# Optimization experiments

Hardware: AMD Instinct MI355X
Metric: run time of the kernel (lower is better)

Reference implementation:

```python
import jax, jax.numpy as jnp
import numpy as np
import math

B, T, C, H = 2, 2048, 1024, 16
HD = C // H  # head_dim = 64
SCALE = 1.0 / math.sqrt(HD)


def _e8_head_dirs(n_heads: int) -> np.ndarray:
    # Type-1 E8 roots in original generation order: (+-1 at i, +-1 at j), i<j,
    # sign order (-1,-1),(-1,1),(1,-1),(1,1); then L2-normalized (norm sqrt(2)).
    roots = []
    for i in range(8):
        for j in range(i + 1, 8):
            for si in (-1.0, 1.0):
                for sj in (-1.0, 1.0):
                    r = np.zeros(8, dtype=np.float32)
                    r[i] = si
                    r[j] = sj
                    roots.append(r)
    roots = np.stack(roots)  # [112, 8], first n_heads used
    roots = roots / np.linalg.norm(roots, axis=1, keepdims=True)
    return roots[:n_heads]


def setup_inputs() -> dict:
    key = jax.random.key(0)
    k1, k2, k3, k4 = jax.random.split(key, 4)
    x = jax.random.normal(k1, (B, T, C), dtype=jnp.float32)
    # nn.Linear-style init scale
    w_qkv = jax.random.normal(k2, (C, 3 * C), dtype=jnp.float32) * (1.0 / math.sqrt(C))
    w_out = jax.random.normal(k3, (C, C), dtype=jnp.float32) * (1.0 / math.sqrt(C))
    head_scales = jax.random.normal(k4, (H,), dtype=jnp.float32) * 0.1
    head_dirs = jnp.asarray(_e8_head_dirs(H))  # [H, 8] buffer (not trained)
    return {"x": x, "w_qkv": w_qkv, "w_out": w_out,
            "head_scales": head_scales, "head_dirs": head_dirs}


def reference(x, w_qkv, w_out, head_scales, head_dirs):
    Bx, Tx, Cx = x.shape
    qkv = (x @ w_qkv).reshape(Bx, Tx, 3, H, HD)
    qkv = jnp.transpose(qkv, (2, 0, 3, 1, 4))  # [3, B, H, T, HD]
    q, k, v = qkv[0], qkv[1], qkv[2]
    scores = jnp.einsum('bhqd,bhkd->bhqk', q, k) * SCALE  # [B,H,T,T]
    causal = jnp.tril(jnp.ones((Tx, Tx), dtype=bool))
    scores = jnp.where(causal[None, None], scores, -jnp.inf)
    # E8 geometric bias: rank-1 per-head bias from projections onto root dirs
    q_proj = jnp.einsum('bhtd,hd->bht', q[..., :8], head_dirs)
    k_proj = jnp.einsum('bhtd,hd->bht', k[..., :8], head_dirs)
    geo_bias = q_proj[..., :, None] * k_proj[..., None, :]  # [B,H,T,T]
    scores = scores + head_scales[None, :, None, None] * geo_bias
    attn = jax.nn.softmax(scores, axis=-1)
    out = jnp.einsum('bhqk,bhkd->bhqd', attn, v)  # [B,H,T,HD]
    out = jnp.transpose(out, (0, 2, 1, 3)).reshape(Bx, Tx, Cx)
    return out @ w_out
```

## Files before the change

kernel.cpp:

```cpp
#include <hip/hip_runtime.h>
#include <stdint.h>


typedef float f32x4 __attribute__((ext_vector_type(4)));
typedef unsigned short u16x8 __attribute__((ext_vector_type(8)));
typedef unsigned short u16x4 __attribute__((ext_vector_type(4)));
typedef unsigned int u32x2 __attribute__((ext_vector_type(2)));
typedef __bf16 bf16x8 __attribute__((ext_vector_type(8)));

static __device__ __forceinline__ unsigned short f2bf(float f) {
  unsigned u = __float_as_uint(f);
  u += 0x7FFFu + ((u >> 16) & 1u);
  return (unsigned short)(u >> 16);
}
static __device__ __forceinline__ float bf2f(unsigned short s) {
  return __uint_as_float(((unsigned)s) << 16);
}
static __device__ __forceinline__ f32x4 mfma16(u16x8 a, u16x8 b, f32x4 c) {
  return __builtin_amdgcn_mfma_f32_16x16x32_bf16(
      __builtin_bit_cast(bf16x8, a), __builtin_bit_cast(bf16x8, b), c, 0, 0, 0);
}
static __device__ __forceinline__ unsigned cvtpk(float lo, float hi) {
  unsigned d;
  asm("v_cvt_pk_bf16_f32 %0, %1, %2" : "=v"(d) : "v"(lo), "v"(hi));
  return d;
}

#define GLD16(gp, lp) __builtin_amdgcn_global_load_lds( \
    (const __attribute__((address_space(1))) unsigned int*)(gp), \
    (__attribute__((address_space(3))) unsigned int*)(lp), 16, 0, 0)

__global__ __launch_bounds__(256) void k_prep(const float* __restrict__ x,
                                              const float* __restrict__ wqkv,
                                              const float* __restrict__ wout,
                                              unsigned short* __restrict__ xb,
                                              unsigned short* __restrict__ wqkvT,
                                              unsigned short* __restrict__ woutT) {
  __shared__ float t[64][65];
  const int bid = blockIdx.x;
  if (bid < 4096) {
    int i = bid * 256 + threadIdx.x;
    f32x4 v = *(const f32x4*)(x + (size_t)i * 4);
    u16x4 o;
#pragma unroll
    for (int j = 0; j < 4; ++j) o[j] = f2bf(v[j]);
    *(u16x4*)(xb + (size_t)i * 4) = o;
    return;
  }
  const float* in;
  unsigned short* out;
  int Cc, bx, by;
  if (bid < 4864) {
    int tt = bid - 4096;
    in = wqkv; out = wqkvT; Cc = 3072;
    bx = tt % 48; by = tt / 48;
  } else {
    int tt = bid - 4864;
    in = wout; out = woutT; Cc = 1024;
    bx = tt & 15; by = tt >> 4;
  }
  const int R = 1024;
  int tr = by * 64, tc = bx * 64;
  int tx = threadIdx.x & 15, ty = threadIdx.x >> 4;
#pragma unroll
  for (int i = 0; i < 4; ++i) {
    int rr = ty + i * 16;
    f32x4 v = *(const f32x4*)(in + (size_t)(tr + rr) * Cc + tc + tx * 4);
#pragma unroll
    for (int j = 0; j < 4; ++j) t[rr][tx * 4 + j] = v[j];
  }
  __syncthreads();
#pragma unroll
  for (int i = 0; i < 4; ++i) {
    int cc = ty + i * 16;
    int rr = tx * 4;
    u16x4 o;
#pragma unroll
    for (int j = 0; j < 4; ++j) o[j] = f2bf(t[rr + j][cc]);
    *(u16x4*)(out + (size_t)(tc + cc) * R + tr + rr) = o;
  }
}

__global__ __launch_bounds__(256) void k_gemm_qkv(const unsigned short* __restrict__ A,
                                                  const unsigned short* __restrict__ Bt,
                                                  unsigned short* __restrict__ qo,
                                                  unsigned short* __restrict__ ko,
                                                  unsigned short* __restrict__ vTo) {
  __shared__ unsigned short lA[128 * 64];
  __shared__ unsigned short lB[128 * 64];
  const int tid = threadIdx.x;
  const int lane = tid & 63, wid = tid >> 6;
  const int wr = wid >> 1, wc = wid & 1;
  const int r = lane & 15, g = lane >> 4;
  const int mbase = blockIdx.y * 128;
  const int nbase = blockIdx.x * 128;
  const int rsw = (r & 7) << 4;

  f32x4 acc[4][4] = {};

  for (int kt = 0; kt < 16; ++kt) {
    __syncthreads();
#pragma unroll
    for (int p = 0; p < 4; ++p) {
      int L = p * 4096 + tid * 16;
      int row = L >> 7;
      int cb = (L >> 4) & 7;
      int cbg = cb ^ (row & 7);
      GLD16(A + (size_t)(mbase + row) * 1024 + kt * 64 + cbg * 8, lA + (L >> 1));
      GLD16(Bt + (size_t)(nbase + row) * 1024 + kt * 64 + cbg * 8, lB + (L >> 1));
    }
    __syncthreads();
#pragma unroll
    for (int s = 0; s < 2; ++s) {
      u16x8 af[4], bfv[4];
      const int csw = (s * 64 + g * 16) ^ rsw;
#pragma unroll
      for (int m = 0; m < 4; ++m)
        af[m] = *(const u16x8*)((const char*)lA + (wr * 64 + m * 16 + r) * 128 + csw);
#pragma unroll
      for (int n = 0; n < 4; ++n)
        bfv[n] = *(const u16x8*)((const char*)lB + (wc * 64 + n * 16 + r) * 128 + csw);
#pragma unroll
      for (int m = 0; m < 4; ++m)
#pragma unroll
        for (int n = 0; n < 4; ++n) acc[m][n] = mfma16(af[m], bfv[n], acc[m][n]);
    }
  }

#pragma unroll
  for (int m = 0; m < 4; ++m) {
#pragma unroll
    for (int n = 0; n < 4; ++n) {
      int ng = nbase + wc * 64 + n * 16 + r;
      int m0 = mbase + wr * 64 + m * 16 + g * 4;
      int sec = ng >> 10, rem = ng & 1023, hh = rem >> 6, d = rem & 63;
      int b = m0 >> 11, t0 = m0 & 2047;
      size_t bh = (size_t)(b * 16 + hh);
      if (sec == 2) {
        u16x4 o;
#pragma unroll
        for (int e = 0; e < 4; ++e) o[e] = f2bf(acc[m][n][e]);
        *(u16x4*)(vTo + (bh * 64 + d) * 2048 + t0) = o;
      } else {
        unsigned short* dst = (sec == 0 ? qo : ko);
#pragma unroll
        for (int e = 0; e < 4; ++e)
          dst[(bh * 2048 + t0 + e) * 64 + d] = f2bf(acc[m][n][e]);
      }
    }
  }
}

__global__ __launch_bounds__(256) void k_gout(const unsigned short* __restrict__ A,
                                              const unsigned short* __restrict__ Bt,
                                              float* __restrict__ fo) {
  __shared__ unsigned short lA[128 * 64];
  __shared__ unsigned short lB[64 * 64];
  const int tid = threadIdx.x;
  const int lane = tid & 63, wid = tid >> 6;
  const int wr = wid >> 1, wc = wid & 1;
  const int r = lane & 15, g = lane >> 4;
  const int mbase = blockIdx.y * 128;
  const int nbase = blockIdx.x * 64;
  const int rsw = (r & 7) << 4;

  f32x4 acc[4][2] = {};

  for (int kt = 0; kt < 16; ++kt) {
    __syncthreads();
#pragma unroll
    for (int p = 0; p < 4; ++p) {
      int L = p * 4096 + tid * 16;
      int row = L >> 7;
      int cb = (L >> 4) & 7;
      int cbg = cb ^ (row & 7);
      GLD16(A + (size_t)(mbase + row) * 1024 + kt * 64 + cbg * 8, lA + (L >> 1));
      if (p < 2)
        GLD16(Bt + (size_t)(nbase + row) * 1024 + kt * 64 + cbg * 8, lB + (L >> 1));
    }
    __syncthreads();
#pragma unroll
    for (int s = 0; s < 2; ++s) {
      u16x8 af[4], bfv[2];
      const int csw = (s * 64 + g * 16) ^ rsw;
#pragma unroll
      for (int m = 0; m < 4; ++m)
        af[m] = *(const u16x8*)((const char*)lA + (wr * 64 + m * 16 + r) * 128 + csw);
#pragma unroll
      for (int n = 0; n < 2; ++n)
        bfv[n] = *(const u16x8*)((const char*)lB + (wc * 32 + n * 16 + r) * 128 + csw);
#pragma unroll
      for (int m = 0; m < 4; ++m)
#pragma unroll
        for (int n = 0; n < 2; ++n) acc[m][n] = mfma16(af[m], bfv[n], acc[m][n]);
    }
  }

#pragma unroll
  for (int m = 0; m < 4; ++m)
#pragma unroll
    for (int n = 0; n < 2; ++n) {
      int ng = nbase + wc * 32 + n * 16 + r;
      int m0 = mbase + wr * 64 + m * 16 + g * 4;
#pragma unroll
      for (int e = 0; e < 4; ++e)
        fo[(size_t)(m0 + e) * 1024 + ng] = acc[m][n][e];
    }
}

__global__ __launch_bounds__(256, 4) void k_attn(const unsigned short* __restrict__ qb,
                                                 const unsigned short* __restrict__ kb,
                                                 const unsigned short* __restrict__ vTb,
                                                 const float* __restrict__ hsc,
                                                 const float* __restrict__ hdir,
                                                 unsigned short* __restrict__ o2) {
  __shared__ unsigned short lK[2][64 * 64];
  __shared__ unsigned short lV[2][64 * 64];
  __shared__ unsigned short lP[4][16 * 64];

  const int tid = threadIdx.x, lane = tid & 63, wid = tid >> 6;
  const int r = lane & 15, g = lane >> 4;
  const int bid = blockIdx.x;
  const int u = bid & 255, kq = bid >> 8;
  const int bh = u & 31, j = u >> 5;
  const int a = (kq == 0) ? j : (kq == 1) ? (31 - j) : (kq == 2) ? (8 + j) : (23 - j);
  const int nk = a + 1;
  const int qbase = a * 64;
  const int h = bh & 15, bi = bh >> 4;

  const size_t kbase = (size_t)bh * (2048 * 64);
  const size_t vbase = (size_t)bh * (64 * 2048);

  const int L0 = tid * 16, L1 = 4096 + tid * 16;
  const int sr0 = L0 >> 7, sr1 = L1 >> 7;
  const int sc0 = ((L0 >> 4) & 7) ^ (sr0 & 7);
  const int sc1 = ((L1 >> 4) & 7) ^ (sr1 & 7);
  const unsigned short* kG0 = kb + kbase + (size_t)sr0 * 64 + sc0 * 8;
  const unsigned short* kG1 = kb + kbase + (size_t)sr1 * 64 + sc1 * 8;
  const unsigned short* vG0 = vTb + vbase + (size_t)sr0 * 2048 + sc0 * 8;
  const unsigned short* vG1 = vTb + vbase + (size_t)sr1 * 2048 + sc1 * 8;
  unsigned short* const dK0a = (unsigned short*)lK[0] + (L0 >> 1);
  unsigned short* const dK0b = (unsigned short*)lK[0] + (L1 >> 1);
  unsigned short* const dK1a = (unsigned short*)lK[1] + (L0 >> 1);
  unsigned short* const dK1b = (unsigned short*)lK[1] + (L1 >> 1);
  unsigned short* const dV0a = (unsigned short*)lV[0] + (L0 >> 1);
  unsigned short* const dV0b = (unsigned short*)lV[0] + (L1 >> 1);
  unsigned short* const dV1a = (unsigned short*)lV[1] + (L0 >> 1);
  unsigned short* const dV1b = (unsigned short*)lV[1] + (L1 >> 1);

#define ATTN_STAGE(B) do {                        \
    GLD16(kG0, dK##B##a); GLD16(kG1, dK##B##b);   \
    GLD16(vG0, dV##B##a); GLD16(vG1, dV##B##b);   \
    kG0 += 4096; kG1 += 4096; vG0 += 64; vG1 += 64; } while (0)

  ATTN_STAGE(0);

  const float LOG2E = 1.44269504088896f;
  const float hs = hsc[h];
  float dir8[8];
#pragma unroll
  for (int j2 = 0; j2 < 8; ++j2) dir8[j2] = hdir[h * 8 + j2];

  u16x8 qc0, qc1;
  {
    const unsigned short* qrow = qb + ((size_t)bh * 2048 + qbase + wid * 16 + r) * 64;
    float proj = 0.f;
    u16x8 qv = *(const u16x8*)qrow;
#pragma unroll
    for (int j2 = 0; j2 < 8; ++j2) proj += bf2f(qv[j2]) * dir8[j2];
#pragma unroll
    for (int s = 0; s < 2; ++s) {
      u16x8 raw = *(const u16x8*)(qrow + s * 32 + g * 8);
      u16x8 ov;
#pragma unroll
      for (int j2 = 0; j2 < 8; ++j2) {
        float v = bf2f(raw[j2]) * (0.125f * LOG2E);
        if (s == 0 && g == 0) v += (hs * LOG2E) * proj * dir8[j2];
        ov[j2] = f2bf(v);
      }
      if (s == 0) qc0 = ov; else qc1 = ov;
    }
  }

  const int swz = (r & 7) << 4;
  const u16x8* kp[2][8];
  const u16x8* vp[2][8];
#pragma unroll
  for (int b = 0; b < 2; ++b) {
    const char* kc = (const char*)lK[b];
    const char* vc = (const char*)lV[b];
#pragma unroll
    for (int ct = 0; ct < 4; ++ct) {
      int krow = ct * 16 + r, sw = (krow & 7) << 4;
      kp[b][ct * 2 + 0] = (const u16x8*)(kc + krow * 128 + ((g * 16) ^ sw));
      kp[b][ct * 2 + 1] = (const u16x8*)(kc + krow * 128 + ((64 + g * 16) ^ sw));
    }
#pragma unroll
    for (int s = 0; s < 2; ++s)
#pragma unroll
      for (int dt = 0; dt < 4; ++dt) {
        int dd = dt * 16 + r;
        vp[b][s * 4 + dt] = (const u16x8*)(vc + dd * 128 + ((s * 64 + g * 16) ^ ((dd & 7) << 4)));
      }
  }
  unsigned short* pw = &lP[wid][0];
  u32x2* pwr[4];
  const u16x8* prd[2];
#pragma unroll
  for (int ct = 0; ct < 4; ++ct)
    pwr[ct] = (u32x2*)((char*)pw + r * 128 + ((ct * 32 + g * 8) ^ swz));
#pragma unroll
  for (int s = 0; s < 2; ++s)
    prd[s] = (const u16x8*)((const char*)pw + r * 128 + ((s * 64 + g * 16) ^ swz));

  f32x4 accO[4] = {};
  float lp = 0.f;
  const int qq = qbase + wid * 16 + r;

  asm volatile("s_waitcnt vmcnt(0)" ::: "memory");
  __builtin_amdgcn_sched_barrier(0);
  __builtin_amdgcn_s_barrier();

#define ATTN_BODY(B, KT) do {                                                  \
    f32x4 accS[4];                                                             \
    __builtin_amdgcn_s_setprio(1);                                             \
    _Pragma("unroll")                                                          \
    for (int ct = 0; ct < 4; ++ct) {                                           \
      f32x4 s4 = {0.f, 0.f, 0.f, 0.f};                                         \
      s4 = mfma16(*kp[B][ct * 2 + 0], qc0, s4);                                \
      s4 = mfma16(*kp[B][ct * 2 + 1], qc1, s4);                                \
      accS[ct] = s4;                                                           \
    }                                                                          \
    __builtin_amdgcn_s_setprio(0);                                             \
    if ((KT) == nk - 1) {                                                      \
      _Pragma("unroll")                                                        \
      for (int ct = 0; ct < 4; ++ct)                                           \
        _Pragma("unroll")                                                      \
        for (int e = 0; e < 4; ++e) {                                          \
          int kk = (KT) * 64 + ct * 16 + g * 4 + e;                            \
          if (kk > qq) accS[ct][e] = -1e30f;                                   \
        }                                                                      \
    }                                                                          \
    float p[4][4];                                                             \
    _Pragma("unroll")                                                          \
    for (int ct = 0; ct < 4; ++ct)                                             \
      _Pragma("unroll")                                                        \
      for (int e = 0; e < 4; ++e) p[ct][e] = exp2f(accS[ct][e]);               \
    _Pragma("unroll")                                                          \
    for (int ct = 0; ct < 4; ++ct)                                             \
      lp += (p[ct][0] + p[ct][1]) + (p[ct][2] + p[ct][3]);                     \
    _Pragma("unroll")                                                          \
    for (int ct = 0; ct < 4; ++ct) {                                           \
      u32x2 w;                                                                 \
      w[0] = cvtpk(p[ct][0], p[ct][1]);                                        \
      w[1] = cvtpk(p[ct][2], p[ct][3]);                                        \
      *pwr[ct] = w;                                                            \
    }                                                                          \
    asm volatile("s_waitcnt lgkmcnt(0)" ::: "memory");                         \
    __builtin_amdgcn_sched_barrier(0);                                         \
    __builtin_amdgcn_s_setprio(1);                                             \
    _Pragma("unroll")                                                          \
    for (int s = 0; s < 2; ++s) {                                              \
      u16x8 pa = *prd[s];                                                      \
      _Pragma("unroll")                                                        \
      for (int dt = 0; dt < 4; ++dt)                                           \
        accO[dt] = mfma16(*vp[B][s * 4 + dt], pa, accO[dt]);                   \
    }                                                                          \
    __builtin_amdgcn_s_setprio(0);                                             \
  } while (0)

#define ATTN_SYNC() do {                                  \
    asm volatile("s_waitcnt vmcnt(0)" ::: "memory");      \
    __builtin_amdgcn_sched_barrier(0);                    \
    __builtin_amdgcn_s_barrier(); } while (0)

  int kt = 0;
  for (;;) {
    if (kt + 1 < nk) ATTN_STAGE(1);
    ATTN_BODY(0, kt);
    ++kt; if (kt == nk) break;
    ATTN_SYNC();
    if (kt + 1 < nk) ATTN_STAGE(0);
    ATTN_BODY(1, kt);
    ++kt; if (kt == nk) break;
    ATTN_SYNC();
  }
#undef ATTN_BODY
#undef ATTN_STAGE
#undef ATTN_SYNC

  lp += __shfl_xor(lp, 16, 64);
  lp += __shfl_xor(lp, 32, 64);
  float inv = 1.f / lp;
#pragma unroll
  for (int dt = 0; dt < 4; ++dt) {
    u16x4 o;
#pragma unroll
    for (int e = 0; e < 4; ++e) o[e] = f2bf(accO[dt][e] * inv);
    *(u16x4*)(o2 + ((size_t)(bi * 2048 + qq)) * 1024 + h * 64 + dt * 16 + g * 4) = o;
  }
}

extern "C" void kernel_launch(void* const* d_in, const int* in_sizes, int n_in,
                              void* d_out, int out_size, void* d_ws, size_t ws_size,
                              hipStream_t stream) {
  const float* x    = (const float*)d_in[0];
  const float* wqkv = (const float*)d_in[1];
  const float* wout = (const float*)d_in[2];
  const float* hsc  = (const float*)d_in[3];
  const float* hdir = (const float*)d_in[4];
  float* outp = (float*)d_out;

  char* ws = (char*)d_ws;
  unsigned short* xb    = (unsigned short*)(ws + 0);
  unsigned short* wqkvT = (unsigned short*)(ws + 8388608);
  unsigned short* woutT = (unsigned short*)(ws + 14680064);
  unsigned short* qb    = (unsigned short*)(ws + 16777216);
  unsigned short* kb    = (unsigned short*)(ws + 25165824);
  unsigned short* vT    = (unsigned short*)(ws + 33554432);
  unsigned short* x2b   = (unsigned short*)(ws + 41943040);
  if (ws_size < 50331648u) return;

  k_prep<<<5120, 256, 0, stream>>>(x, wqkv, wout, xb, wqkvT, woutT);
  k_gemm_qkv<<<dim3(24, 32), 256, 0, stream>>>(xb, wqkvT, qb, kb, vT);
  k_attn<<<dim3(1024), 256, 0, stream>>>(qb, kb, vT, hsc, hdir, x2b);
  k_gout<<<dim3(16, 32), 256, 0, stream>>>(x2b, woutT, outp);
}
```

Before: 99.07 us.

## Feed softmax probabilities to PV MFMA directly from registers, dropping LDS P round-trip

Removes the per-wave LDS staging buffer for the probability tile. Each lane now packs its own exp2 results from the S accumulator layout straight into the B operand of the PV MFMA. To keep the reduction dimension consistent, V is read from LDS as two 8-byte halves matching the permuted key order. This removes an LDS write, a wait and a read per tile, and frees shared memory, at the cost of twice as many narrower V reads from LDS.

```diff
diff --git a/kernel.cpp b/kernel.cpp
--- a/kernel.cpp
+++ b/kernel.cpp
@@ -6,6 +6,7 @@
 typedef unsigned short u16x8 __attribute__((ext_vector_type(8)));
 typedef unsigned short u16x4 __attribute__((ext_vector_type(4)));
 typedef unsigned int u32x2 __attribute__((ext_vector_type(2)));
+typedef unsigned int u32x4 __attribute__((ext_vector_type(4)));
 typedef __bf16 bf16x8 __attribute__((ext_vector_type(8)));
 
 static __device__ __forceinline__ unsigned short f2bf(float f) {
@@ -216,7 +217,6 @@
                                                  unsigned short* __restrict__ o2) {
   __shared__ unsigned short lK[2][64 * 64];
   __shared__ unsigned short lV[2][64 * 64];
-  __shared__ unsigned short lP[4][16 * 64];
 
   const int tid = threadIdx.x, lane = tid & 63, wid = tid >> 6;
   const int r = lane & 15, g = lane >> 4;
@@ -282,9 +282,8 @@
     }
   }
 
-  const int swz = (r & 7) << 4;
   const u16x8* kp[2][8];
-  const u16x8* vp[2][8];
+  const u16x4* vk[2][16];
 #pragma unroll
   for (int b = 0; b < 2; ++b) {
     const char* kc = (const char*)lK[b];
@@ -296,22 +295,14 @@
       kp[b][ct * 2 + 1] = (const u16x8*)(kc + krow * 128 + ((64 + g * 16) ^ sw));
     }
 #pragma unroll
-    for (int s = 0; s < 2; ++s)
+    for (int ct = 0; ct < 4; ++ct)
 #pragma unroll
       for (int dt = 0; dt < 4; ++dt) {
         int dd = dt * 16 + r;
-        vp[b][s * 4 + dt] = (const u16x8*)(vc + dd * 128 + ((s * 64 + g * 16) ^ ((dd & 7) << 4)));
+        vk[b][ct * 4 + dt] =
+            (const u16x4*)(vc + dd * 128 + ((ct * 32 + g * 8) ^ ((dd & 7) << 4)));
       }
   }
-  unsigned short* pw = &lP[wid][0];
-  u32x2* pwr[4];
-  const u16x8* prd[2];
-#pragma unroll
-  for (int ct = 0; ct < 4; ++ct)
-    pwr[ct] = (u32x2*)((char*)pw + r * 128 + ((ct * 32 + g * 8) ^ swz));
-#pragma unroll
-  for (int s = 0; s < 2; ++s)
-    prd[s] = (const u16x8*)((const char*)pw + r * 128 + ((s * 64 + g * 16) ^ swz));
 
   f32x4 accO[4] = {};
   float lp = 0.f;
@@ -341,30 +332,28 @@
           if (kk > qq) accS[ct][e] = -1e30f;                                   \
         }                                                                      \
     }                                                                          \
-    float p[4][4];                                                             \
-    _Pragma("unroll")                                                          \
-    for (int ct = 0; ct < 4; ++ct)                                             \
-      _Pragma("unroll")                                                        \
-      for (int e = 0; e < 4; ++e) p[ct][e] = exp2f(accS[ct][e]);               \
-    _Pragma("unroll")                                                          \
-    for (int ct = 0; ct < 4; ++ct)                                             \
-      lp += (p[ct][0] + p[ct][1]) + (p[ct][2] + p[ct][3]);                     \
-    _Pragma("unroll")                                                          \
-    for (int ct = 0; ct < 4; ++ct) {                                           \
-      u32x2 w;                                                                 \
-      w[0] = cvtpk(p[ct][0], p[ct][1]);                                        \
-      w[1] = cvtpk(p[ct][2], p[ct][3]);                                        \
-      *pwr[ct] = w;                                                            \
-    }                                                                          \
-    asm volatile("s_waitcnt lgkmcnt(0)" ::: "memory");                         \
-    __builtin_amdgcn_sched_barrier(0);                                         \
     __builtin_amdgcn_s_setprio(1);                                             \
     _Pragma("unroll")                                                          \
-    for (int s = 0; s < 2; ++s) {                                              \
-      u16x8 pa = *prd[s];                                                      \
+    for (int cp = 0; cp < 2; ++cp) {                                           \
+      const int c0 = cp * 2, c1 = cp * 2 + 1;                                  \
+      float a0 = exp2f(accS[c0][0]), a1 = exp2f(accS[c0][1]);                  \
+      float a2 = exp2f(accS[c0][2]), a3 = exp2f(accS[c0][3]);                  \
+      float b0 = exp2f(accS[c1][0]), b1 = exp2f(accS[c1][1]);                  \
+      float b2 = exp2f(accS[c1][2]), b3 = exp2f(accS[c1][3]);                  \
+      lp += ((a0 + a1) + (a2 + a3)) + ((b0 + b1) + (b2 + b3));                 \
+      u32x4 wp;                                                                \
+      wp[0] = cvtpk(a0, a1);                                                   \
+      wp[1] = cvtpk(a2, a3);                                                   \
+      wp[2] = cvtpk(b0, b1);                                                   \
+      wp[3] = cvtpk(b2, b3);                                                   \
+      u16x8 pa = __builtin_bit_cast(u16x8, wp);                                \
       _Pragma("unroll")                                                        \
-      for (int dt = 0; dt < 4; ++dt)                                           \
-        accO[dt] = mfma16(*vp[B][s * 4 + dt], pa, accO[dt]);                   \
+      for (int dt = 0; dt < 4; ++dt) {                                         \
+        u16x4 lo = *vk[B][c0 * 4 + dt];                                        \
+        u16x4 hi = *vk[B][c1 * 4 + dt];                                        \
+        u16x8 vv = __builtin_shufflevector(lo, hi, 0, 1, 2, 3, 4, 5, 6, 7);    \
+        accO[dt] = mfma16(vv, pa, accO[dt]);                                   \
+      }                                                                        \
     }                                                                          \
     __builtin_amdgcn_s_setprio(0);                                             \
   } while (0)
```

After: 100.5 us. Within noise of the previous version (+1.4%).

## Triple-buffer K/V in attention and software-pipeline next-tile QK^T

Applied to the files above, without the earlier changes.

The attention kernel moves from double to triple LDS buffering of K/V tiles, prefetching two tiles ahead. It also computes the QK^T scores for the next tile before the softmax and PV of the current one, so MFMA work overlaps the exp and LDS traffic. The extra LDS and registers lead to launch bounds being lowered from 4 to 2 blocks per CU, which reduces occupancy.

```diff
diff --git a/kernel.cpp b/kernel.cpp
--- a/kernel.cpp
+++ b/kernel.cpp
@@ -208,14 +208,14 @@
     }
 }
 
-__global__ __launch_bounds__(256, 4) void k_attn(const unsigned short* __restrict__ qb,
+__global__ __launch_bounds__(256, 2) void k_attn(const unsigned short* __restrict__ qb,
                                                  const unsigned short* __restrict__ kb,
                                                  const unsigned short* __restrict__ vTb,
                                                  const float* __restrict__ hsc,
                                                  const float* __restrict__ hdir,
                                                  unsigned short* __restrict__ o2) {
-  __shared__ unsigned short lK[2][64 * 64];
-  __shared__ unsigned short lV[2][64 * 64];
+  __shared__ unsigned short lK[3][64 * 64];
+  __shared__ unsigned short lV[3][64 * 64];
   __shared__ unsigned short lP[4][16 * 64];
 
   const int tid = threadIdx.x, lane = tid & 63, wid = tid >> 6;
@@ -239,21 +239,23 @@
   const unsigned short* kG1 = kb + kbase + (size_t)sr1 * 64 + sc1 * 8;
   const unsigned short* vG0 = vTb + vbase + (size_t)sr0 * 2048 + sc0 * 8;
   const unsigned short* vG1 = vTb + vbase + (size_t)sr1 * 2048 + sc1 * 8;
-  unsigned short* const dK0a = (unsigned short*)lK[0] + (L0 >> 1);
-  unsigned short* const dK0b = (unsigned short*)lK[0] + (L1 >> 1);
-  unsigned short* const dK1a = (unsigned short*)lK[1] + (L0 >> 1);
-  unsigned short* const dK1b = (unsigned short*)lK[1] + (L1 >> 1);
-  unsigned short* const dV0a = (unsigned short*)lV[0] + (L0 >> 1);
-  unsigned short* const dV0b = (unsigned short*)lV[0] + (L1 >> 1);
-  unsigned short* const dV1a = (unsigned short*)lV[1] + (L0 >> 1);
-  unsigned short* const dV1b = (unsigned short*)lV[1] + (L1 >> 1);
-
-#define ATTN_STAGE(B) do {                        \
-    GLD16(kG0, dK##B##a); GLD16(kG1, dK##B##b);   \
-    GLD16(vG0, dV##B##a); GLD16(vG1, dV##B##b);   \
+  unsigned short* dKd[3][2];
+  unsigned short* dVd[3][2];
+#pragma unroll
+  for (int b = 0; b < 3; ++b) {
+    dKd[b][0] = (unsigned short*)lK[b] + (L0 >> 1);
+    dKd[b][1] = (unsigned short*)lK[b] + (L1 >> 1);
+    dVd[b][0] = (unsigned short*)lV[b] + (L0 >> 1);
+    dVd[b][1] = (unsigned short*)lV[b] + (L1 >> 1);
+  }
+
+#define ATTN_STAGE(B) do {                          \
+    GLD16(kG0, dKd[B][0]); GLD16(kG1, dKd[B][1]);   \
+    GLD16(vG0, dVd[B][0]); GLD16(vG1, dVd[B][1]);   \
     kG0 += 4096; kG1 += 4096; vG0 += 64; vG1 += 64; } while (0)
 
   ATTN_STAGE(0);
+  if (nk > 1) ATTN_STAGE(1);
 
   const float LOG2E = 1.44269504088896f;
   const float hs = hsc[h];
@@ -283,10 +285,10 @@
   }
 
   const int swz = (r & 7) << 4;
-  const u16x8* kp[2][8];
-  const u16x8* vp[2][8];
-#pragma unroll
-  for (int b = 0; b < 2; ++b) {
+  const u16x8* kp[3][8];
+  const u16x8* vp[3][8];
+#pragma unroll
+  for (int b = 0; b < 3; ++b) {
     const char* kc = (const char*)lK[b];
     const char* vc = (const char*)lV[b];
 #pragma unroll
@@ -314,6 +316,7 @@
     prd[s] = (const u16x8*)((const char*)pw + r * 128 + ((s * 64 + g * 16) ^ swz));
 
   f32x4 accO[4] = {};
+  f32x4 sc[4] = {}, sn[4] = {};
   float lp = 0.f;
   const int qq = qbase + wid * 16 + r;
 
@@ -321,31 +324,37 @@
   __builtin_amdgcn_sched_barrier(0);
   __builtin_amdgcn_s_barrier();
 
-#define ATTN_BODY(B, KT) do {                                                  \
-    f32x4 accS[4];                                                             \
+#define ATTN_QK(B, DST) do {                                                   \
     __builtin_amdgcn_s_setprio(1);                                             \
     _Pragma("unroll")                                                          \
     for (int ct = 0; ct < 4; ++ct) {                                           \
       f32x4 s4 = {0.f, 0.f, 0.f, 0.f};                                         \
       s4 = mfma16(*kp[B][ct * 2 + 0], qc0, s4);                                \
       s4 = mfma16(*kp[B][ct * 2 + 1], qc1, s4);                                \
-      accS[ct] = s4;                                                           \
+      DST[ct] = s4;                                                            \
     }                                                                          \
     __builtin_amdgcn_s_setprio(0);                                             \
-    if ((KT) == nk - 1) {                                                      \
+  } while (0)
+
+  ATTN_QK(0, sc);
+
+#define ATTN_BODY(CB, NB, SB) do {                                             \
+    if (t + 2 < nk) ATTN_STAGE(SB);                                            \
+    if (t + 1 < nk) ATTN_QK(NB, sn);                                           \
+    if (t == nk - 1) {                                                         \
       _Pragma("unroll")                                                        \
       for (int ct = 0; ct < 4; ++ct)                                           \
         _Pragma("unroll")                                                      \
         for (int e = 0; e < 4; ++e) {                                          \
-          int kk = (KT) * 64 + ct * 16 + g * 4 + e;                            \
-          if (kk > qq) accS[ct][e] = -1e30f;                                   \
+          int kk = t * 64 + ct * 16 + g * 4 + e;                               \
+          if (kk > qq) sc[ct][e] = -1e30f;                                     \
         }                                                                      \
     }                                                                          \
     float p[4][4];                                                             \
     _Pragma("unroll")                                                          \
     for (int ct = 0; ct < 4; ++ct)                                             \
       _Pragma("unroll")                                                        \
-      for (int e = 0; e < 4; ++e) p[ct][e] = exp2f(accS[ct][e]);               \
+      for (int e = 0; e < 4; ++e) p[ct][e] = exp2f(sc[ct][e]);                 \
     _Pragma("unroll")                                                          \
     for (int ct = 0; ct < 4; ++ct)                                             \
       lp += (p[ct][0] + p[ct][1]) + (p[ct][2] + p[ct][3]);                     \
@@ -364,30 +373,30 @@
       u16x8 pa = *prd[s];                                                      \
       _Pragma("unroll")                                                        \
       for (int dt = 0; dt < 4; ++dt)                                           \
-        accO[dt] = mfma16(*vp[B][s * 4 + dt], pa, accO[dt]);                   \
+        accO[dt] = mfma16(*vp[CB][s * 4 + dt], pa, accO[dt]);                  \
     }                                                                          \
     __builtin_amdgcn_s_setprio(0);                                             \
+    _Pragma("unroll")                                                          \
+    for (int ct = 0; ct < 4; ++ct) sc[ct] = sn[ct];                            \
+    if (t + 1 < nk) {                                                          \
+      asm volatile("s_waitcnt vmcnt(0)" ::: "memory");                         \
+      __builtin_amdgcn_sched_barrier(0);                                       \
+      __builtin_amdgcn_s_barrier();                                            \
+    }                                                                          \
   } while (0)
 
-#define ATTN_SYNC() do {                                  \
-    asm volatile("s_waitcnt vmcnt(0)" ::: "memory");      \
-    __builtin_amdgcn_sched_barrier(0);                    \
-    __builtin_amdgcn_s_barrier(); } while (0)
-
-  int kt = 0;
+  int t = 0;
   for (;;) {
-    if (kt + 1 < nk) ATTN_STAGE(1);
-    ATTN_BODY(0, kt);
-    ++kt; if (kt == nk) break;
-    ATTN_SYNC();
-    if (kt + 1 < nk) ATTN_STAGE(0);
-    ATTN_BODY(1, kt);
-    ++kt; if (kt == nk) break;
-    ATTN_SYNC();
+    ATTN_BODY(0, 1, 2);
+    ++t; if (t == nk) break;
+    ATTN_BODY(1, 2, 0);
+    ++t; if (t == nk) break;
+    ATTN_BODY(2, 0, 1);
+    ++t; if (t == nk) break;
   }
 #undef ATTN_BODY
+#undef ATTN_QK
 #undef ATTN_STAGE
-#undef ATTN_SYNC
 
   lp += __shfl_xor(lp, 16, 64);
   lp += __shfl_xor(lp, 32, 64);
```

Result: slower. 105.2 us (+6.2%).
